# Kernel optimization log

Measured on AMD Instinct MI355X. Metric: run time of the kernel, lower is better.

The kernel has to match this reference:

```python
import jax, jax.numpy as jnp
import numpy as np

HEAD_SIZE = 64
N_EMBED = 1024
B, T = 8, 2048


def setup_inputs() -> dict:
    key = jax.random.key(0)
    ks = jax.random.split(key, 7)
    s = lambda fan_in: 1.0 / np.sqrt(fan_in)
    return {
        "x": jax.random.normal(ks[0], (B, T, N_EMBED), dtype=jnp.float32),
        # Linear weights stored as (in, out) so projection is x @ W + b
        "Wk": jax.random.uniform(ks[1], (N_EMBED, HEAD_SIZE), jnp.float32, -s(N_EMBED), s(N_EMBED)),
        "bk": jax.random.uniform(ks[2], (HEAD_SIZE,), jnp.float32, -s(N_EMBED), s(N_EMBED)),
        "Wq": jax.random.uniform(ks[3], (N_EMBED, HEAD_SIZE), jnp.float32, -s(N_EMBED), s(N_EMBED)),
        "bq": jax.random.uniform(ks[4], (HEAD_SIZE,), jnp.float32, -s(N_EMBED), s(N_EMBED)),
        "Wv": jax.random.uniform(ks[5], (N_EMBED, HEAD_SIZE), jnp.float32, -s(N_EMBED), s(N_EMBED)),
        "bv": jax.random.uniform(ks[6], (HEAD_SIZE,), jnp.float32, -s(N_EMBED), s(N_EMBED)),
    }


def reference(x, Wk, bk, Wq, bq, Wv, bv):
    Bb, Tt, C = x.shape
    k = x @ Wk + bk  # [B,T,H]
    q = x @ Wq + bq
    v = x @ Wv + bv
    # NOTE: original computes k @ q^T (keys as rows, queries as cols)
    wei = jnp.einsum("bth,bsh->bts", k, q) * (C ** -0.5)  # [B,T,T]
    causal = jnp.tril(jnp.ones((Tt, Tt), dtype=bool))
    wei = jnp.where(causal, wei, -jnp.inf)
    # softplus instead of softmax; softplus(-inf) = 0, stable via logaddexp
    wei = jnp.logaddexp(wei, 0.0)
    # dropout omitted (eval mode / deterministic reference)
    out = jnp.einsum("bts,bsh->bth", wei, v)  # [B,T,H]
    return out
```

## Files before the change

kernel.cpp:

```cpp
#include <hip/hip_runtime.h>
#include <hip/hip_bf16.h>
#include <stdint.h>

#define HEAD 64
#define CEMB 1024
#define BB 8
#define TSEQ 2048

typedef __attribute__((ext_vector_type(8))) short bf16x8;
typedef __attribute__((ext_vector_type(4))) float f32x4;

__device__ __forceinline__ unsigned short f2bf(float f) {
    union { float f; uint32_t u; } c; c.f = f;
    uint32_t u = c.u + 0x7FFF + ((c.u >> 16) & 1);
    return (unsigned short)(u >> 16);
}
__device__ __forceinline__ ushort4 f4bf(float4 v) {
    ushort4 u; u.x = f2bf(v.x); u.y = f2bf(v.y); u.z = f2bf(v.z); u.w = f2bf(v.w);
    return u;
}

__global__ __launch_bounds__(256) void prep_w(
        const float* __restrict__ Wk, const float* __restrict__ bk,
        const float* __restrict__ Wq, const float* __restrict__ bq,
        const float* __restrict__ Wv, const float* __restrict__ bv,
        unsigned short* __restrict__ WTf, float* __restrict__ biasb) {
    __shared__ float Wl[3][32][64];
    const int kc = blockIdx.x;
    const int tid = threadIdx.x;
    const float* Ws[3] = {Wk, Wq, Wv};
    const int row = tid >> 3, cf = (tid & 7) * 8;
    #pragma unroll
    for (int p = 0; p < 3; p++) {
        const float* W = Ws[p] + (long)(kc * 32 + row) * 64 + cf;
        float4 v0 = *(const float4*)(W);
        float4 v1 = *(const float4*)(W + 4);
        *(float4*)(&Wl[p][row][cf]) = v0;
        *(float4*)(&Wl[p][row][cf + 4]) = v1;
    }
    __syncthreads();
    #pragma unroll
    for (int i = 0; i < 3; i++) {
        int cid = i * 256 + tid;
        int lane = cid & 63;
        int l15 = lane & 15, q4 = lane >> 4;
        int n = (cid >> 6) * 16 + l15;
        int p = n >> 6, col = n & 63;
        float scale = (p == 1) ? 0.03125f : 1.0f;
        unsigned short o[8];
        for (int e = 0; e < 8; e++) o[e] = f2bf(Wl[p][q4 * 8 + e][col] * scale);
        *(int4*)(WTf + (long)kc * 6144 + (long)cid * 8) = *(int4*)o;
    }
    if (kc == 0 && tid < 192) {
        const float* bs[3] = {bk, bq, bv};
        int p = tid >> 6;
        biasb[tid] = bs[p][tid & 63] * ((p == 1) ? 0.03125f : 1.0f);
    }
}

__global__ __launch_bounds__(768) void proj_gemm(
        const float* __restrict__ x, const unsigned short* __restrict__ WTf,
        const float* __restrict__ biasb,
        unsigned short* __restrict__ Kb, unsigned short* __restrict__ Qb,
        unsigned short* __restrict__ VTb) {
    __shared__ __align__(16) unsigned short As[64 * 1032];

    const int tid = threadIdx.x;
    const int lane = tid & 63, w = tid >> 6;
    const int l15 = lane & 15, q4 = lane >> 4;
    const long rowbase = (long)blockIdx.x * 64;
    const float* xg = x + rowbase * CEMB;
    const unsigned short* Bg = WTf + w * 512 + (long)lane * 8;

    f32x4 z = {0.f, 0.f, 0.f, 0.f};
    f32x4 acc[4];
    #pragma unroll
    for (int m = 0; m < 4; m++) acc[m] = z;

    bf16x8 Breg[16];

    {
        #pragma unroll
        for (int it = 0; it < 3; it++) {
            int i = it * 768 + tid;
            if (i < 2048) {
                int row = i >> 5, c4 = (i & 31) * 4;
                float4 v = *(const float4*)(xg + row * CEMB + c4);
                *(ushort4*)(As + row * 1032 + c4) = f4bf(v);
            }
        }
    }
    __syncthreads();

    #pragma unroll
    for (int half = 0; half < 2; half++) {
        #pragma unroll
        for (int i = 0; i < 16; i++)
            Breg[i] = *(const bf16x8*)(Bg + (long)(half * 16 + i) * 6144);

        #pragma unroll
        for (int ss = 0; ss < 4; ss++) {
            const int s = half * 4 + ss;
            float4 pf[3];
            if (s < 7) {
                #pragma unroll
                for (int it = 0; it < 3; it++) {
                    int i = it * 768 + tid;
                    if (i < 2048) {
                        int row = i >> 5, c4 = (i & 31) * 4;
                        pf[it] = *(const float4*)(xg + row * CEMB + (s + 1) * 128 + c4);
                    }
                }
            }
            #pragma unroll
            for (int kc = 0; kc < 4; kc++) {
                const int kg = s * 4 + kc;
                #pragma unroll
                for (int m = 0; m < 4; m++) {
                    bf16x8 a = *(const bf16x8*)(As + (m * 16 + l15) * 1032 + kg * 32 + q4 * 8);
                    acc[m] = __builtin_amdgcn_mfma_f32_16x16x32_bf16(a, Breg[ss * 4 + kc], acc[m], 0, 0, 0);
                }
            }
            if (s < 7) {
                #pragma unroll
                for (int it = 0; it < 3; it++) {
                    int i = it * 768 + tid;
                    if (i < 2048) {
                        int row = i >> 5, c4 = (i & 31) * 4;
                        *(ushort4*)(As + row * 1032 + (s + 1) * 128 + c4) = f4bf(pf[it]);
                    }
                }
                __syncthreads();
            }
        }
    }

    const int n = w * 16 + l15;
    const float bias = biasb[n];
    #pragma unroll
    for (int m = 0; m < 4; m++) {
        const long row0 = rowbase + m * 16 + q4 * 4;
        if (n < 128) {
            unsigned short* dst = (n < 64) ? (Kb + row0 * HEAD + n)
                                           : (Qb + row0 * HEAD + (n - 64));
            for (int r = 0; r < 4; r++)
                dst[r * HEAD] = f2bf(acc[m][r] + bias);
        } else {
            const int h = n - 128;
            const long b = row0 >> 11; const int t = (int)(row0 & 2047);
            ushort4 pk;
            pk.x = f2bf(acc[m][0] + bias);
            pk.y = f2bf(acc[m][1] + bias);
            pk.z = f2bf(acc[m][2] + bias);
            pk.w = f2bf(acc[m][3] + bias);
            *(ushort4*)(VTb + b * (HEAD * (long)TSEQ) + (long)h * TSEQ + t) = pk;
        }
    }
}

__global__ __launch_bounds__(512) void attn(
        const unsigned short* __restrict__ Kb, const unsigned short* __restrict__ Qb,
        const unsigned short* __restrict__ VTb, float* __restrict__ out) {
    __shared__ __align__(16) char sm[36864];
    unsigned short* Pl = (unsigned short*)sm;
    float* red = (float*)sm;

    const int tid = threadIdx.x;
    const int lane = tid & 63, w = tid >> 6;
    const int l15 = lane & 15, q4 = lane >> 4;

    const int bid = blockIdx.x;
    const int half = bid >> 8;
    const int slot = (bid & 255) >> 3;
    const int ti = half ? slot : 63 - slot;
    const int b = bid & 7;
    const int t0 = ti * 32;

    const unsigned short* kb  = Kb  + (long)b * TSEQ * HEAD;
    const unsigned short* qb  = Qb  + (long)b * TSEQ * HEAD;
    const unsigned short* vtb = VTb + (long)b * HEAD * TSEQ;

    bf16x8 kf[2][2];
    for (int tt = 0; tt < 2; tt++)
        for (int kk = 0; kk < 2; kk++)
            kf[tt][kk] = *(const bf16x8*)(kb + (t0 + tt * 16 + l15) * HEAD + kk * 32 + q4 * 8);

    f32x4 z = {0.f, 0.f, 0.f, 0.f};
    f32x4 oacc[4][2];
    for (int hh = 0; hh < 4; hh++) for (int tt = 0; tt < 2; tt++) oacc[hh][tt] = z;

    bf16x8 qpf[2][2], vpf[4];
    if (w <= ti) {
        const int s0 = w * 32;
        for (int st2 = 0; st2 < 2; st2++)
            for (int kk = 0; kk < 2; kk++)
                qpf[st2][kk] = *(const bf16x8*)(qb + (s0 + st2 * 16 + l15) * HEAD + kk * 32 + q4 * 8);
        for (int hh = 0; hh < 4; hh++)
            vpf[hh] = *(const bf16x8*)(vtb + (hh * 16 + l15) * (long)TSEQ + s0 + q4 * 8);
    }

    unsigned short* myP = Pl + w * 1280;
    for (int c = w; c <= ti; c += 8) {
        const int s0 = c * 32;

        bf16x8 qf[2][2], vf[4];
        for (int st2 = 0; st2 < 2; st2++)
            for (int kk = 0; kk < 2; kk++) qf[st2][kk] = qpf[st2][kk];
        for (int hh = 0; hh < 4; hh++) vf[hh] = vpf[hh];

        if (c + 8 <= ti) {
            const int sn = (c + 8) * 32;
            for (int st2 = 0; st2 < 2; st2++)
                for (int kk = 0; kk < 2; kk++)
                    qpf[st2][kk] = *(const bf16x8*)(qb + (sn + st2 * 16 + l15) * HEAD + kk * 32 + q4 * 8);
            for (int hh = 0; hh < 4; hh++)
                vpf[hh] = *(const bf16x8*)(vtb + (hh * 16 + l15) * (long)TSEQ + sn + q4 * 8);
        }

        f32x4 sc[2][2];
        for (int st2 = 0; st2 < 2; st2++)
            for (int tt = 0; tt < 2; tt++) {
                f32x4 s = z;
                s = __builtin_amdgcn_mfma_f32_16x16x32_bf16(qf[st2][0], kf[tt][0], s, 0, 0, 0);
                s = __builtin_amdgcn_mfma_f32_16x16x32_bf16(qf[st2][1], kf[tt][1], s, 0, 0, 0);
                sc[st2][tt] = s;
            }
        for (int tt = 0; tt < 2; tt++) {
            const int tg = t0 + tt * 16 + l15;
            for (int st2 = 0; st2 < 2; st2++) {
                ushort4 pk;
                unsigned short pv[4];
                for (int r = 0; r < 4; r++) {
                    int sg = s0 + st2 * 16 + q4 * 4 + r;
                    float p = __logf(1.0f + __expf(sc[st2][tt][r]));
                    if (sg > tg) p = 0.0f;
                    pv[r] = f2bf(p);
                }
                pk.x = pv[0]; pk.y = pv[1]; pk.z = pv[2]; pk.w = pv[3];
                *(ushort4*)(myP + (tt * 16 + l15) * 40 + st2 * 16 + q4 * 4) = pk;
            }
        }
        asm volatile("s_waitcnt lgkmcnt(0)" ::: "memory");
        bf16x8 pf0 = *(const bf16x8*)(myP + l15 * 40 + q4 * 8);
        bf16x8 pf1 = *(const bf16x8*)(myP + (16 + l15) * 40 + q4 * 8);
        for (int hh = 0; hh < 4; hh++) {
            oacc[hh][0] = __builtin_amdgcn_mfma_f32_16x16x32_bf16(vf[hh], pf0, oacc[hh][0], 0, 0, 0);
            oacc[hh][1] = __builtin_amdgcn_mfma_f32_16x16x32_bf16(vf[hh], pf1, oacc[hh][1], 0, 0, 0);
        }
    }

    __syncthreads();
    if (w >= 4) {
        float* r0 = red + (w - 4) * 2304 + lane * 36;
        for (int hh = 0; hh < 4; hh++)
            for (int tt = 0; tt < 2; tt++)
                *(f32x4*)(r0 + (hh * 2 + tt) * 4) = oacc[hh][tt];
    }
    __syncthreads();
    if (w < 4) {
        const float* r0 = red + w * 2304 + lane * 36;
        for (int hh = 0; hh < 4; hh++)
            for (int tt = 0; tt < 2; tt++)
                oacc[hh][tt] += *(const f32x4*)(r0 + (hh * 2 + tt) * 4);
    }
    __syncthreads();
    if (w == 2 || w == 3) {
        float* r0 = red + (w - 2) * 2304 + lane * 36;
        for (int hh = 0; hh < 4; hh++)
            for (int tt = 0; tt < 2; tt++)
                *(f32x4*)(r0 + (hh * 2 + tt) * 4) = oacc[hh][tt];
    }
    __syncthreads();
    if (w < 2) {
        const float* r0 = red + w * 2304 + lane * 36;
        for (int hh = 0; hh < 4; hh++)
            for (int tt = 0; tt < 2; tt++)
                oacc[hh][tt] += *(const f32x4*)(r0 + (hh * 2 + tt) * 4);
    }
    __syncthreads();
    if (w == 1) {
        float* r0 = red + lane * 36;
        for (int hh = 0; hh < 4; hh++)
            for (int tt = 0; tt < 2; tt++)
                *(f32x4*)(r0 + (hh * 2 + tt) * 4) = oacc[hh][tt];
    }
    __syncthreads();
    if (w == 0) {
        const float* r0 = red + lane * 36;
        for (int hh = 0; hh < 4; hh++)
            for (int tt = 0; tt < 2; tt++)
                oacc[hh][tt] += *(const f32x4*)(r0 + (hh * 2 + tt) * 4);
        for (int tt = 0; tt < 2; tt++) {
            float* ob = out + ((long)b * TSEQ + t0 + tt * 16 + l15) * HEAD + q4 * 4;
            for (int hh = 0; hh < 4; hh++)
                *(f32x4*)(ob + hh * 16) = oacc[hh][tt];
        }
    }
}

extern "C" void kernel_launch(void* const* d_in, const int* in_sizes, int n_in,
                              void* d_out, int out_size, void* d_ws, size_t ws_size,
                              hipStream_t stream) {
    const float* x  = (const float*)d_in[0];
    const float* Wk = (const float*)d_in[1];
    const float* bk = (const float*)d_in[2];
    const float* Wq = (const float*)d_in[3];
    const float* bq = (const float*)d_in[4];
    const float* Wv = (const float*)d_in[5];
    const float* bv = (const float*)d_in[6];
    float* out = (float*)d_out;

    char* ws = (char*)d_ws;
    unsigned short* WTf   = (unsigned short*)(ws);
    float*          biasb = (float*)(ws + 393216);
    unsigned short* Kb    = (unsigned short*)(ws + 524288);
    unsigned short* Qb    = (unsigned short*)(ws + 524288 + 2097152);
    unsigned short* VTb   = (unsigned short*)(ws + 524288 + 4194304);

    prep_w<<<32, 256, 0, stream>>>(Wk, bk, Wq, bq, Wv, bv, WTf, biasb);
    proj_gemm<<<256, 768, 0, stream>>>(x, WTf, biasb, Kb, Qb, VTb);
    attn<<<512, 512, 0, stream>>>(Kb, Qb, VTb, out);
}
```

Baseline: 145.9 us.

## Retile projection GEMM to 32-row blocks with double-buffered LDS and streamed weights

The projection GEMM moves from 256 blocks of 768 threads, each holding a full 64x1024 bf16 row tile in LDS, to 512 blocks of 384 threads. Each block now covers 32 rows, double-buffers 128-column chunks of x in a small LDS ring, and each wave computes two 16-column output tiles. Weight fragments are prefetched per K-chunk into alternating register sets instead of loading 16 fragments at a time. The aim is to cut LDS usage so several blocks fit per CU and to spread work over more CUs. In exchange, each block reads the weights for only half as many rows, so total weight traffic per row doubles.

```diff
diff --git a/kernel.cpp b/kernel.cpp
--- a/kernel.cpp
+++ b/kernel.cpp
@@ -58,102 +58,116 @@
     }
 }
 
-__global__ __launch_bounds__(768) void proj_gemm(
+__global__ __launch_bounds__(384, 3) void proj_gemm(
         const float* __restrict__ x, const unsigned short* __restrict__ WTf,
         const float* __restrict__ biasb,
         unsigned short* __restrict__ Kb, unsigned short* __restrict__ Qb,
         unsigned short* __restrict__ VTb) {
-    __shared__ __align__(16) unsigned short As[64 * 1032];
+    __shared__ __align__(16) unsigned short As[2][32][136];
 
     const int tid = threadIdx.x;
     const int lane = tid & 63, w = tid >> 6;
     const int l15 = lane & 15, q4 = lane >> 4;
-    const long rowbase = (long)blockIdx.x * 64;
+    const long rowbase = (long)blockIdx.x * 32;
     const float* xg = x + rowbase * CEMB;
-    const unsigned short* Bg = WTf + w * 512 + (long)lane * 8;
+    const unsigned short* Bg = WTf + (2 * w) * 512 + (long)lane * 8;
 
     f32x4 z = {0.f, 0.f, 0.f, 0.f};
-    f32x4 acc[4];
-    #pragma unroll
-    for (int m = 0; m < 4; m++) acc[m] = z;
-
-    bf16x8 Breg[16];
+    f32x4 acc[2][2];
+    #pragma unroll
+    for (int nt = 0; nt < 2; nt++)
+        #pragma unroll
+        for (int m = 0; m < 2; m++) acc[nt][m] = z;
+
+    bf16x8 Bb0[2][4], Bb1[2][4];
 
     {
         #pragma unroll
         for (int it = 0; it < 3; it++) {
-            int i = it * 768 + tid;
-            if (i < 2048) {
+            int i = it * 384 + tid;
+            if (i < 1024) {
                 int row = i >> 5, c4 = (i & 31) * 4;
                 float4 v = *(const float4*)(xg + row * CEMB + c4);
-                *(ushort4*)(As + row * 1032 + c4) = f4bf(v);
-            }
-        }
-    }
-    __syncthreads();
-
-    #pragma unroll
-    for (int half = 0; half < 2; half++) {
-        #pragma unroll
-        for (int i = 0; i < 16; i++)
-            Breg[i] = *(const bf16x8*)(Bg + (long)(half * 16 + i) * 6144);
-
-        #pragma unroll
-        for (int ss = 0; ss < 4; ss++) {
-            const int s = half * 4 + ss;
-            float4 pf[3];
-            if (s < 7) {
+                *(ushort4*)(&As[0][row][c4]) = f4bf(v);
+            }
+        }
+        #pragma unroll
+        for (int nt = 0; nt < 2; nt++)
+            #pragma unroll
+            for (int kc = 0; kc < 4; kc++)
+                Bb0[nt][kc] = *(const bf16x8*)(Bg + (long)nt * 512 + (long)kc * 6144);
+    }
+    __syncthreads();
+
+    #pragma unroll
+    for (int s = 0; s < 8; s++) {
+        float4 pf[3];
+        if (s < 7) {
+            #pragma unroll
+            for (int it = 0; it < 3; it++) {
+                int i = it * 384 + tid;
+                if (i < 1024) {
+                    int row = i >> 5, c4 = (i & 31) * 4;
+                    pf[it] = *(const float4*)(xg + row * CEMB + (s + 1) * 128 + c4);
+                }
+            }
+            #pragma unroll
+            for (int nt = 0; nt < 2; nt++)
                 #pragma unroll
-                for (int it = 0; it < 3; it++) {
-                    int i = it * 768 + tid;
-                    if (i < 2048) {
-                        int row = i >> 5, c4 = (i & 31) * 4;
-                        pf[it] = *(const float4*)(xg + row * CEMB + (s + 1) * 128 + c4);
-                    }
-                }
-            }
-            #pragma unroll
-            for (int kc = 0; kc < 4; kc++) {
-                const int kg = s * 4 + kc;
-                #pragma unroll
-                for (int m = 0; m < 4; m++) {
-                    bf16x8 a = *(const bf16x8*)(As + (m * 16 + l15) * 1032 + kg * 32 + q4 * 8);
-                    acc[m] = __builtin_amdgcn_mfma_f32_16x16x32_bf16(a, Breg[ss * 4 + kc], acc[m], 0, 0, 0);
-                }
-            }
-            if (s < 7) {
-                #pragma unroll
-                for (int it = 0; it < 3; it++) {
-                    int i = it * 768 + tid;
-                    if (i < 2048) {
-                        int row = i >> 5, c4 = (i & 31) * 4;
-                        *(ushort4*)(As + row * 1032 + (s + 1) * 128 + c4) = f4bf(pf[it]);
-                    }
-                }
-                __syncthreads();
-            }
-        }
-    }
-
-    const int n = w * 16 + l15;
-    const float bias = biasb[n];
-    #pragma unroll
-    for (int m = 0; m < 4; m++) {
-        const long row0 = rowbase + m * 16 + q4 * 4;
-        if (n < 128) {
-            unsigned short* dst = (n < 64) ? (Kb + row0 * HEAD + n)
-                                           : (Qb + row0 * HEAD + (n - 64));
-            for (int r = 0; r < 4; r++)
-                dst[r * HEAD] = f2bf(acc[m][r] + bias);
-        } else {
-            const int h = n - 128;
-            const long b = row0 >> 11; const int t = (int)(row0 & 2047);
-            ushort4 pk;
-            pk.x = f2bf(acc[m][0] + bias);
-            pk.y = f2bf(acc[m][1] + bias);
-            pk.z = f2bf(acc[m][2] + bias);
-            pk.w = f2bf(acc[m][3] + bias);
-            *(ushort4*)(VTb + b * (HEAD * (long)TSEQ) + (long)h * TSEQ + t) = pk;
+                for (int kc = 0; kc < 4; kc++) {
+                    bf16x8 v = *(const bf16x8*)(Bg + (long)nt * 512 + (long)((s + 1) * 4 + kc) * 6144);
+                    if (s & 1) Bb0[nt][kc] = v; else Bb1[nt][kc] = v;
+                }
+        }
+        #pragma unroll
+        for (int kc = 0; kc < 4; kc++) {
+            #pragma unroll
+            for (int m = 0; m < 2; m++) {
+                bf16x8 a = *(const bf16x8*)(&As[s & 1][m * 16 + l15][kc * 32 + q4 * 8]);
+                if (s & 1) {
+                    acc[0][m] = __builtin_amdgcn_mfma_f32_16x16x32_bf16(a, Bb1[0][kc], acc[0][m], 0, 0, 0);
+                    acc[1][m] = __builtin_amdgcn_mfma_f32_16x16x32_bf16(a, Bb1[1][kc], acc[1][m], 0, 0, 0);
+                } else {
+                    acc[0][m] = __builtin_amdgcn_mfma_f32_16x16x32_bf16(a, Bb0[0][kc], acc[0][m], 0, 0, 0);
+                    acc[1][m] = __builtin_amdgcn_mfma_f32_16x16x32_bf16(a, Bb0[1][kc], acc[1][m], 0, 0, 0);
+                }
+            }
+        }
+        if (s < 7) {
+            #pragma unroll
+            for (int it = 0; it < 3; it++) {
+                int i = it * 384 + tid;
+                if (i < 1024) {
+                    int row = i >> 5, c4 = (i & 31) * 4;
+                    *(ushort4*)(&As[(s & 1) ^ 1][row][c4]) = f4bf(pf[it]);
+                }
+            }
+            __syncthreads();
+        }
+    }
+
+    #pragma unroll
+    for (int nt = 0; nt < 2; nt++) {
+        const int n = (2 * w + nt) * 16 + l15;
+        const float bias = biasb[n];
+        #pragma unroll
+        for (int m = 0; m < 2; m++) {
+            const long row0 = rowbase + m * 16 + q4 * 4;
+            if (n < 128) {
+                unsigned short* dst = (n < 64) ? (Kb + row0 * HEAD + n)
+                                               : (Qb + row0 * HEAD + (n - 64));
+                for (int r = 0; r < 4; r++)
+                    dst[r * HEAD] = f2bf(acc[nt][m][r] + bias);
+            } else {
+                const int h = n - 128;
+                const long b = row0 >> 11; const int t = (int)(row0 & 2047);
+                ushort4 pk;
+                pk.x = f2bf(acc[nt][m][0] + bias);
+                pk.y = f2bf(acc[nt][m][1] + bias);
+                pk.z = f2bf(acc[nt][m][2] + bias);
+                pk.w = f2bf(acc[nt][m][3] + bias);
+                *(ushort4*)(VTb + b * (HEAD * (long)TSEQ) + (long)h * TSEQ + t) = pk;
+            }
         }
     }
 }
@@ -318,6 +332,6 @@
     unsigned short* VTb   = (unsigned short*)(ws + 524288 + 4194304);
 
     prep_w<<<32, 256, 0, stream>>>(Wk, bk, Wq, bq, Wv, bv, WTf, biasb);
-    proj_gemm<<<256, 768, 0, stream>>>(x, WTf, biasb, Kb, Qb, VTb);
+    proj_gemm<<<512, 384, 0, stream>>>(x, WTf, biasb, Kb, Qb, VTb);
     attn<<<512, 512, 0, stream>>>(Kb, Qb, VTb, out);
 }
```

Result: no change. 144.8 us (-0.7%).
